# Kernel tuning notes

Measured on AMD Instinct MI355X. Metric: run time of the kernel, lower is better.

## Reference

```python
import jax, jax.numpy as jnp
import numpy as np

K = 3
STRIDE = 1
PADDING = 1
INVALID = -1.0


def _unfold(x, k, stride, padding, fill):
    # x: [B, C, H, W] -> patches [B, C, k, k, P] matching torch F.unfold ordering
    x = jnp.pad(x, ((0, 0), (0, 0), (padding, padding), (padding, padding)),
                constant_values=fill)
    # feature dim ordered channel-major (C, kh, kw), same as torch unfold
    p = jax.lax.conv_general_dilated_patches(x, (k, k), (stride, stride), 'VALID')
    b, _, ho, wo = p.shape
    c = x.shape[1]
    return p.reshape(b, c, k, k, ho * wo), ho, wo


def setup_inputs() -> dict:
    key = jax.random.key(0)
    k1, k2, k3, k4 = jax.random.split(key, 4)
    B, C, H, W = 8, 64, 128, 128
    OC = 64
    inp = jax.random.normal(k1, (B, C, H, W), dtype=jnp.float32)
    mask = jax.random.randint(k2, (B, H, W), 0, 4).astype(jnp.float32)
    conv = jax.random.normal(k3, (OC, C, K, K), dtype=jnp.float32) * 0.05
    bias = jax.random.normal(k4, (OC,), dtype=jnp.float32) * 0.05
    return {"inp": inp, "mask": mask, "conv": conv, "bias": bias}


def reference(inp, mask, conv, bias):
    k, stride, padding = K, STRIDE, PADDING
    b, c, h_in, w_in = inp.shape
    oc = conv.shape[0]
    center = (k - 1) // 2

    inp_patched, ho, wo = _unfold(inp, k, stride, padding, INVALID)       # [B,C,k,k,P]
    mask_patched, _, _ = _unfold(mask[:, None], k, stride, padding, INVALID)  # [B,1,k,k,P]
    mask_patched = mask_patched[:, 0]                                      # [B,k,k,P]

    center_val = mask_patched[:, center:center + 1, center:center + 1, :]  # [B,1,1,P]
    mask_eq = (mask_patched == center_val).astype(inp.dtype)               # [B,k,k,P]

    masked_input = inp_patched * mask_eq[:, None]                          # [B,C,k,k,P]
    m_norm = (k * k) / jnp.clip(mask_eq.reshape(b, k * k, -1).sum(axis=1), 1e-8)  # [B,P]

    masked_input = masked_input.reshape(b, c, k * k, -1)                   # [B,C,kk,P]
    w = conv.reshape(oc, c, k * k)                                         # [O,C,kk]
    out = jnp.einsum('bcxp,ocx->bop', masked_input, w)                     # [B,O,P]
    out = out * m_norm[:, None, :]
    out = out.reshape(b, oc, ho, wo)
    out = out + bias[None, :, None, None]

    mask_out = mask_patched[:, center, center, :].reshape(b, 1, ho, wo)
    return out, mask_out
```

## Files before the change

kernel.cpp:

```cpp
#include <hip/hip_runtime.h>
#include <stdint.h>

#define HW   128
#define CIN  64
#define OCN  64
#define NB   8

typedef __attribute__((ext_vector_type(8)))  short short8;
typedef __attribute__((ext_vector_type(16))) float floatx16;

union F8 { short8 s; uint32_t d[4]; uint4 q; };

static __device__ __forceinline__ ushort f2bf(float f) {
    uint32_t u = __float_as_uint(f);
    return (ushort)((u + 0x7FFFu + ((u >> 16) & 1u)) >> 16);
}

__global__ __launch_bounds__(256)
void prep_kernel(const float* __restrict__ inp, const float* __restrict__ conv,
                 ushort* __restrict__ wb, ushort* __restrict__ xb)
{
    const int bid = blockIdx.x, tid = threadIdx.x;
    if (bid >= 1024) {
        int t = bid - 1024;
        #pragma unroll
        for (int i = 0; i < 16; ++i) {
            int id = i * 256 + tid;
            int oc = id >> 6, c = id & 63;
            wb[t * 4096 + id] = f2bf(conv[(oc * 64 + c) * 9 + t]);
        }
        return;
    }
    const int bb = bid >> 7, y = bid & 127;
    const int cg = tid & 7;
    const int xg = tid >> 3;
    const float* src = inp + ((size_t)(bb * CIN + cg * 8) * HW + y) * HW + xg * 4;
    float4 v[8];
    #pragma unroll
    for (int k = 0; k < 8; ++k)
        v[k] = *(const float4*)(src + (size_t)k * HW * HW);
    const float* fv = (const float*)v;
    ushort* dst = xb + (size_t)(bb * HW + y) * HW * 64;
    #pragma unroll
    for (int j = 0; j < 4; ++j) {
        int px = xg * 4 + j;
        uint32_t d0 = (uint32_t)f2bf(fv[0 * 4 + j]) | ((uint32_t)f2bf(fv[1 * 4 + j]) << 16);
        uint32_t d1 = (uint32_t)f2bf(fv[2 * 4 + j]) | ((uint32_t)f2bf(fv[3 * 4 + j]) << 16);
        uint32_t d2 = (uint32_t)f2bf(fv[4 * 4 + j]) | ((uint32_t)f2bf(fv[5 * 4 + j]) << 16);
        uint32_t d3 = (uint32_t)f2bf(fv[6 * 4 + j]) | ((uint32_t)f2bf(fv[7 * 4 + j]) << 16);
        int slot = cg ^ (px & 7);
        *(uint4*)(dst + px * 64 + slot * 8) = make_uint4(d0, d1, d2, d3);
    }
}

#define LDS_BYTES 65536

__global__ __launch_bounds__(256, 2)
void iconv_main(const ushort* __restrict__ xb, const ushort* __restrict__ wb,
                const float* __restrict__ mask, const float* __restrict__ bias,
                float* __restrict__ out)
{
    extern __shared__ char smem[];
    ushort* Ls = (ushort*)smem;

    const int tid  = threadIdx.x;
    const int bb   = blockIdx.x >> 6;
    const int y0   = (blockIdx.x & 63) << 1;
    const int lane = tid & 63, l31 = lane & 31, lh = lane >> 5;
    const int w    = tid >> 6;
    const int yloc = w >> 1, xh = w & 1;
    const int y    = y0 + yloc, xw = xh * 64;
    const int x0   = xw + l31, x1 = x0 + 32;

    {
        int gy = y0 - 1 + w;
        gy = gy < 0 ? 0 : (gy > HW - 1 ? HW - 1 : gy);
        const ushort* grow = xb + ((size_t)(bb * HW + gy) * HW) * 64;
        ushort* lrow = Ls + w * 8192;
        #pragma unroll
        for (int i = 0; i < 16; ++i) {
            __builtin_amdgcn_global_load_lds(
                (const __attribute__((address_space(1))) uint32_t*)(grow + i * 512 + lane * 8),
                (__attribute__((address_space(3))) uint32_t*)(lrow + i * 512),
                16, 0, 0);
        }
    }

    const float* mrow = mask + ((size_t)bb * HW + y) * HW;
    const float m00 = mrow[x0], m01 = mrow[x1];
    uint32_t bits0 = 0, bits1 = 0;
    #pragma unroll
    for (int t = 0; t < 9; ++t) {
        int dy = t / 3 - 1, dx = t % 3 - 1;
        int ny = y + dy;
        bool vy = (ny >= 0) && (ny < HW);
        int nyc = vy ? ny : y;
        const float* r = mask + ((size_t)bb * HW + nyc) * HW;
        int nx0 = x0 + dx, nx1 = x1 + dx;
        bool ok0 = vy && (nx0 >= 0) && (nx0 < HW);
        bool ok1 = vy && (nx1 >= 0) && (nx1 < HW);
        int c0 = nx0 < 0 ? 0 : (nx0 > HW - 1 ? HW - 1 : nx0);
        int c1 = nx1 < 0 ? 0 : (nx1 > HW - 1 ? HW - 1 : nx1);
        if (ok0 && r[c0] == m00) bits0 |= 1u << t;
        if (ok1 && r[c1] == m01) bits1 |= 1u << t;
    }
    const float norm0 = 9.0f / (float)__popc(bits0);
    const float norm1 = 9.0f / (float)__popc(bits1);

    float* mout = out + (size_t)NB * OCN * HW * HW + ((size_t)bb * HW + y) * HW;
    mout[x0] = m00;
    mout[x1] = m01;

    uint4 Ar[2][8];
    #pragma unroll
    for (int i = 0; i < 8; ++i) {
        int h = i >> 2, ks = i & 3;
        Ar[0][i] = *(const uint4*)(wb + (l31 + h * 32) * 64 + ks * 16 + lh * 8);
    }

    __syncthreads();

    floatx16 acc00 = {0,0,0,0,0,0,0,0,0,0,0,0,0,0,0,0};
    floatx16 acc01 = {0,0,0,0,0,0,0,0,0,0,0,0,0,0,0,0};
    floatx16 acc10 = {0,0,0,0,0,0,0,0,0,0,0,0,0,0,0,0};
    floatx16 acc11 = {0,0,0,0,0,0,0,0,0,0,0,0,0,0,0,0};

    #pragma unroll
    for (int t = 0; t < 9; ++t) {
        const int buf = t & 1;
        if (t < 8) {
            const ushort* wp = wb + (t + 1) * 4096;
            #pragma unroll
            for (int i = 0; i < 8; ++i) {
                int h = i >> 2, ks = i & 3;
                Ar[buf ^ 1][i] = *(const uint4*)(wp + (l31 + h * 32) * 64 + ks * 16 + lh * 8);
            }
        }

        const int dy = t / 3 - 1, dx = t % 3 - 1;
        const int rrB = 1 + yloc + dy;
        int p0 = x0 + dx; p0 = p0 < 0 ? 0 : (p0 > HW - 1 ? HW - 1 : p0);
        int p1 = x1 + dx; p1 = p1 < 0 ? 0 : (p1 > HW - 1 ? HW - 1 : p1);
        const ushort* b0b = Ls + rrB * 8192 + p0 * 64;
        const ushort* b1b = Ls + rrB * 8192 + p1 * 64;
        const int sw0 = p0 & 7, sw1 = p1 & 7;
        const uint32_t s0 = ((bits0 >> t) & 1u) ? 0xFFFFFFFFu : 0u;
        const uint32_t s1 = ((bits1 >> t) & 1u) ? 0xFFFFFFFFu : 0u;

        #pragma unroll
        for (int ks = 0; ks < 4; ++ks) {
            F8 a0, a1, b0, b1;
            a0.q = Ar[buf][ks];
            a1.q = Ar[buf][4 + ks];
            b0.q = *(const uint4*)(b0b + (((2 * ks + lh) ^ sw0) * 8));
            b1.q = *(const uint4*)(b1b + (((2 * ks + lh) ^ sw1) * 8));
            b0.d[0] &= s0; b0.d[1] &= s0; b0.d[2] &= s0; b0.d[3] &= s0;
            b1.d[0] &= s1; b1.d[1] &= s1; b1.d[2] &= s1; b1.d[3] &= s1;
            acc00 = __builtin_amdgcn_mfma_f32_32x32x16_bf16(a0.s, b0.s, acc00, 0, 0, 0);
            acc01 = __builtin_amdgcn_mfma_f32_32x32x16_bf16(a0.s, b1.s, acc01, 0, 0, 0);
            acc10 = __builtin_amdgcn_mfma_f32_32x32x16_bf16(a1.s, b0.s, acc10, 0, 0, 0);
            acc11 = __builtin_amdgcn_mfma_f32_32x32x16_bf16(a1.s, b1.s, acc11, 0, 0, 0);
        }
    }

    float* outp = out + (size_t)bb * OCN * HW * HW + (size_t)y * HW;
    #pragma unroll
    for (int mt = 0; mt < 2; ++mt) {
        #pragma unroll
        for (int nt = 0; nt < 2; ++nt) {
            floatx16 a = (mt == 0) ? (nt == 0 ? acc00 : acc01)
                                   : (nt == 0 ? acc10 : acc11);
            float nm = (nt == 0) ? norm0 : norm1;
            int x = xw + nt * 32 + l31;
            #pragma unroll
            for (int r = 0; r < 16; ++r) {
                int oc = mt * 32 + (r & 3) + 8 * (r >> 2) + 4 * lh;
                outp[(size_t)oc * (HW * HW) + x] = a[r] * nm + bias[oc];
            }
        }
    }
}

extern "C" void kernel_launch(void* const* d_in, const int* in_sizes, int n_in,
                              void* d_out, int out_size, void* d_ws, size_t ws_size,
                              hipStream_t stream) {
    (void)in_sizes; (void)n_in; (void)out_size; (void)ws_size;
    const float* inp  = (const float*)d_in[0];
    const float* mask = (const float*)d_in[1];
    const float* conv = (const float*)d_in[2];
    const float* bias = (const float*)d_in[3];
    float* out = (float*)d_out;

    ushort* wb = (ushort*)d_ws;
    ushort* xb = (ushort*)d_ws + 65536;

    hipFuncSetAttribute((const void*)iconv_main,
                        hipFuncAttributeMaxDynamicSharedMemorySize, LDS_BYTES);

    prep_kernel<<<1033, 256, 0, stream>>>(inp, conv, wb, xb);
    iconv_main<<<NB * (HW / 2), 256, LDS_BYTES, stream>>>(xb, wb, mask, bias, out);
}
```

Measured before the change: 117.3 us.

## Fuse input bf16 conversion into conv kernel and pre-swizzle weights

```diff
diff --git a/kernel.cpp b/kernel.cpp
--- a/kernel.cpp
+++ b/kernel.cpp
@@ -17,46 +17,22 @@
 }
 
 __global__ __launch_bounds__(256)
-void prep_kernel(const float* __restrict__ inp, const float* __restrict__ conv,
-                 ushort* __restrict__ wb, ushort* __restrict__ xb)
-{
-    const int bid = blockIdx.x, tid = threadIdx.x;
-    if (bid >= 1024) {
-        int t = bid - 1024;
-        #pragma unroll
-        for (int i = 0; i < 16; ++i) {
-            int id = i * 256 + tid;
-            int oc = id >> 6, c = id & 63;
-            wb[t * 4096 + id] = f2bf(conv[(oc * 64 + c) * 9 + t]);
-        }
-        return;
-    }
-    const int bb = bid >> 7, y = bid & 127;
-    const int cg = tid & 7;
-    const int xg = tid >> 3;
-    const float* src = inp + ((size_t)(bb * CIN + cg * 8) * HW + y) * HW + xg * 4;
-    float4 v[8];
-    #pragma unroll
-    for (int k = 0; k < 8; ++k)
-        v[k] = *(const float4*)(src + (size_t)k * HW * HW);
-    const float* fv = (const float*)v;
-    ushort* dst = xb + (size_t)(bb * HW + y) * HW * 64;
-    #pragma unroll
-    for (int j = 0; j < 4; ++j) {
-        int px = xg * 4 + j;
-        uint32_t d0 = (uint32_t)f2bf(fv[0 * 4 + j]) | ((uint32_t)f2bf(fv[1 * 4 + j]) << 16);
-        uint32_t d1 = (uint32_t)f2bf(fv[2 * 4 + j]) | ((uint32_t)f2bf(fv[3 * 4 + j]) << 16);
-        uint32_t d2 = (uint32_t)f2bf(fv[4 * 4 + j]) | ((uint32_t)f2bf(fv[5 * 4 + j]) << 16);
-        uint32_t d3 = (uint32_t)f2bf(fv[6 * 4 + j]) | ((uint32_t)f2bf(fv[7 * 4 + j]) << 16);
-        int slot = cg ^ (px & 7);
-        *(uint4*)(dst + px * 64 + slot * 8) = make_uint4(d0, d1, d2, d3);
-    }
+void wprep_kernel(const float* __restrict__ conv, ushort* __restrict__ wb2) {
+    int idx = blockIdx.x * 256 + threadIdx.x;
+    int j  = idx & 7;
+    int l  = (idx >> 3) & 63;
+    int h  = (idx >> 9) & 1;
+    int ks = (idx >> 10) & 3;
+    int t  = idx >> 12;
+    int oc = (l & 31) + h * 32;
+    int c  = ks * 16 + (l >> 5) * 8 + j;
+    wb2[idx] = f2bf(conv[(oc * 64 + c) * 9 + t]);
 }
 
 #define LDS_BYTES 65536
 
 __global__ __launch_bounds__(256, 2)
-void iconv_main(const ushort* __restrict__ xb, const ushort* __restrict__ wb,
+void iconv_main(const float* __restrict__ inp, const ushort* __restrict__ wb2,
                 const float* __restrict__ mask, const float* __restrict__ bias,
                 float* __restrict__ out)
 {
@@ -73,16 +49,28 @@
     const int x0   = xw + l31, x1 = x0 + 32;
 
     {
-        int gy = y0 - 1 + w;
-        gy = gy < 0 ? 0 : (gy > HW - 1 ? HW - 1 : gy);
-        const ushort* grow = xb + ((size_t)(bb * HW + gy) * HW) * 64;
-        ushort* lrow = Ls + w * 8192;
+        const int cg = tid & 7, xg = tid >> 3;
         #pragma unroll
-        for (int i = 0; i < 16; ++i) {
-            __builtin_amdgcn_global_load_lds(
-                (const __attribute__((address_space(1))) uint32_t*)(grow + i * 512 + lane * 8),
-                (__attribute__((address_space(3))) uint32_t*)(lrow + i * 512),
-                16, 0, 0);
+        for (int rr = 0; rr < 4; ++rr) {
+            int gy = y0 - 1 + rr;
+            gy = gy < 0 ? 0 : (gy > HW - 1 ? HW - 1 : gy);
+            const float* src = inp + ((size_t)(bb * CIN + cg * 8) * HW + gy) * HW + xg * 4;
+            float4 v[8];
+            #pragma unroll
+            for (int k = 0; k < 8; ++k)
+                v[k] = *(const float4*)(src + (size_t)k * HW * HW);
+            const float* fv = (const float*)v;
+            ushort* lrow = Ls + rr * 8192;
+            #pragma unroll
+            for (int j = 0; j < 4; ++j) {
+                int px = xg * 4 + j;
+                uint32_t d0 = (uint32_t)f2bf(fv[0 * 4 + j]) | ((uint32_t)f2bf(fv[1 * 4 + j]) << 16);
+                uint32_t d1 = (uint32_t)f2bf(fv[2 * 4 + j]) | ((uint32_t)f2bf(fv[3 * 4 + j]) << 16);
+                uint32_t d2 = (uint32_t)f2bf(fv[4 * 4 + j]) | ((uint32_t)f2bf(fv[5 * 4 + j]) << 16);
+                uint32_t d3 = (uint32_t)f2bf(fv[6 * 4 + j]) | ((uint32_t)f2bf(fv[7 * 4 + j]) << 16);
+                int slot = cg ^ (px & 7);
+                *(uint4*)(lrow + px * 64 + slot * 8) = make_uint4(d0, d1, d2, d3);
+            }
         }
     }
 
@@ -114,8 +102,8 @@
     uint4 Ar[2][8];
     #pragma unroll
     for (int i = 0; i < 8; ++i) {
-        int h = i >> 2, ks = i & 3;
-        Ar[0][i] = *(const uint4*)(wb + (l31 + h * 32) * 64 + ks * 16 + lh * 8);
+        int ks = i >> 1, h = i & 1;
+        Ar[0][h * 4 + ks] = *(const uint4*)(wb2 + (size_t)i * 512 + lane * 8);
     }
 
     __syncthreads();
@@ -129,11 +117,11 @@
     for (int t = 0; t < 9; ++t) {
         const int buf = t & 1;
         if (t < 8) {
-            const ushort* wp = wb + (t + 1) * 4096;
+            const ushort* wp = wb2 + (size_t)(t + 1) * 4096;
             #pragma unroll
             for (int i = 0; i < 8; ++i) {
-                int h = i >> 2, ks = i & 3;
-                Ar[buf ^ 1][i] = *(const uint4*)(wp + (l31 + h * 32) * 64 + ks * 16 + lh * 8);
+                int ks = i >> 1, h = i & 1;
+                Ar[buf ^ 1][h * 4 + ks] = *(const uint4*)(wp + (size_t)i * 512 + lane * 8);
             }
         }
 
@@ -191,12 +179,11 @@
     const float* bias = (const float*)d_in[3];
     float* out = (float*)d_out;
 
-    ushort* wb = (ushort*)d_ws;
-    ushort* xb = (ushort*)d_ws + 65536;
+    ushort* wb2 = (ushort*)d_ws;
 
     hipFuncSetAttribute((const void*)iconv_main,
                         hipFuncAttributeMaxDynamicSharedMemorySize, LDS_BYTES);
 
-    prep_kernel<<<1033, 256, 0, stream>>>(inp, conv, wb, xb);
-    iconv_main<<<NB * (HW / 2), 256, LDS_BYTES, stream>>>(xb, wb, mask, bias, out);
+    wprep_kernel<<<144, 256, 0, stream>>>(conv, wb2);
+    iconv_main<<<NB * (HW / 2), 256, LDS_BYTES, stream>>>(inp, wb2, mask, bias, out);
 }
```

Result: faster. 106.2 us (-9.4%).
